# Kernel optimization log

Hardware: AMD Instinct MI355X
Metric: run time of the kernel (lower is better)

The kernel has to match this reference:

```python
import jax, jax.numpy as jnp
import numpy as np

N = 100000
E = 3200000
D_IN = 128
D_OUT = 128


def setup_inputs() -> dict:
    key = jax.random.key(0)
    k1, k2, k3, k4, k5, k6, k7 = jax.random.split(key, 7)
    stdv = 1.0 / np.sqrt(D_OUT)
    x = jax.random.normal(k1, (N, D_IN), dtype=jnp.float32)
    rows = jax.random.randint(k2, (E,), 0, N, dtype=jnp.int32)
    cols = jax.random.randint(k3, (E,), 0, N, dtype=jnp.int32)
    edge_w = jax.random.uniform(k4, (E,), dtype=jnp.float32)
    W = jax.random.uniform(k5, (D_IN, D_OUT), minval=-stdv, maxval=stdv, dtype=jnp.float32)
    W_skip = jax.random.uniform(k6, (D_IN, D_OUT), minval=-stdv, maxval=stdv, dtype=jnp.float32)
    b = jax.random.uniform(k7, (D_OUT,), minval=-stdv, maxval=stdv, dtype=jnp.float32)
    return {"x": x, "rows": rows, "cols": cols, "edge_w": edge_w,
            "W": W, "W_skip": W_skip, "b": b}


def reference(x, rows, cols, edge_w, W, W_skip, b):
    # support1 = x @ W  [N, D_OUT]
    support1 = jnp.dot(x, W)
    # spmm(norm_adj, support1): out[r] = sum_{(r,c) in E} w_rc * support1[c]
    msgs = support1[cols] * edge_w[:, None]          # [E, D_OUT] gather
    agg = jax.ops.segment_sum(msgs, rows, num_segments=N)  # [N, D_OUT] scatter-add
    # skip connection + bias
    out = agg + jnp.dot(x, W_skip) + b
    return out
```

## Files before the change

kernel.cpp:

```cpp
#include <hip/hip_runtime.h>

#define D 128
#define B_LOG 6
#define ROWS_PB 64
#define MAX_NB 2048
#define GEMM_GRID 784
#define CHUNK_LOG 12
#define CAP 2560

typedef short bf16x8 __attribute__((ext_vector_type(8)));
typedef float f32x4  __attribute__((ext_vector_type(4)));

static __device__ __forceinline__ unsigned short f2bf(float f) {
    unsigned u = __float_as_uint(f);
    u += 0x7FFFu + ((u >> 16) & 1u);
    return (unsigned short)(u >> 16);
}

__global__ __launch_bounds__(256) void wconv_kernel(
    const float* __restrict__ W, const float* __restrict__ Ws,
    short* __restrict__ Wt, int* __restrict__ bhist, int nb)
{
    const int idx = blockIdx.x * 256 + threadIdx.x;
    if (idx < 2 * D * D) {
        const int mat = idx >> 14;
        const int rem = idx & (D * D - 1);
        const int n = rem >> 7, k = rem & (D - 1);
        const float* src = mat ? Ws : W;
        Wt[idx] = (short)f2bf(src[k * D + n]);
    }
    if (idx < nb) bhist[idx] = 0;
}

__global__ __launch_bounds__(256) void bhist_kernel(
    const int* __restrict__ rows, int* __restrict__ bhist, int E, int nb)
{
    __shared__ int h[MAX_NB];
    const int t = threadIdx.x;
    for (int i = t; i < nb; i += 256) h[i] = 0;
    __syncthreads();

    int i = blockIdx.x * 256 + t;
    const int stride = gridDim.x * 256;
    for (; i < E; i += stride) atomicAdd(&h[rows[i] >> B_LOG], 1);
    __syncthreads();

    for (int i2 = t; i2 < nb; i2 += 256) {
        const int c = h[i2];
        if (c) atomicAdd(&bhist[i2], c);
    }
}

__global__ __launch_bounds__(256) void bscan_kernel(
    const int* __restrict__ bhist, int* __restrict__ bptr,
    int* __restrict__ bcur, int nb)
{
    const int t = threadIdx.x;
    const int base_i = t * 8;
    int v[8];
    int s = 0;
#pragma unroll
    for (int k = 0; k < 8; ++k) {
        v[k] = (base_i + k < nb) ? bhist[base_i + k] : 0;
        s += v[k];
    }

    const int lane = t & 63, wv = t >> 6;
    int sc = s;
    for (int o = 1; o < 64; o <<= 1) {
        const int u = __shfl_up(sc, o, 64);
        if (lane >= o) sc += u;
    }
    __shared__ int wsum[4];
    if (lane == 63) wsum[wv] = sc;
    __syncthreads();

    int wbase = 0;
    for (int w2 = 0; w2 < wv; ++w2) wbase += wsum[w2];
    int excl = wbase + (sc - s);
#pragma unroll
    for (int k = 0; k < 8; ++k) {
        if (base_i + k < nb) { bptr[base_i + k] = excl; bcur[base_i + k] = excl; }
        excl += v[k];
    }
    if (t == 255) bptr[nb] = wsum[0] + wsum[1] + wsum[2] + wsum[3];
}

__global__ __launch_bounds__(256) void gemm_part_kernel(
    const float* __restrict__ x, const short* __restrict__ Wt,
    const float* __restrict__ b, unsigned short* __restrict__ s1b,
    unsigned short* __restrict__ skipb, int N,
    const int* __restrict__ rows, const int* __restrict__ cols,
    const float* __restrict__ ew, int* __restrict__ bcur,
    int2* __restrict__ se1, int E, int nb)
{
    __shared__ short sx[64 * D];

    const int t = threadIdx.x;

    if (blockIdx.x >= GEMM_GRID) {
        int* h = (int*)sx;
        const int nbl = gridDim.x - GEMM_GRID;
        const int nchunks = (E + (1 << CHUNK_LOG) - 1) >> CHUNK_LOG;

        for (int c = blockIdx.x - GEMM_GRID; c < nchunks; c += nbl) {
            const int ebeg = c << CHUNK_LOG;
            const int eend = min(ebeg + (1 << CHUNK_LOG), E);

            for (int i = t; i < nb; i += 256) h[i] = 0;
            __syncthreads();

            for (int e = ebeg + t; e < eend; e += 256)
                atomicAdd(&h[rows[e] >> B_LOG], 1);
            __syncthreads();

            for (int i = t; i < nb; i += 256) {
                const int cnt = h[i];
                h[i] = cnt ? atomicAdd(&bcur[i], cnt) : 0;
            }
            __syncthreads();

            for (int e = ebeg + t; e < eend; e += 256) {
                const int r    = rows[e];
                const int bkt  = r >> B_LOG;
                const int slot = atomicAdd(&h[bkt], 1);
                se1[slot] = make_int2(((r & (ROWS_PB - 1)) << 20) | cols[e],
                                      __float_as_int(ew[e]));
            }
            __syncthreads();
        }
        return;
    }

    const int lane = t & 63;
    const int w    = t >> 6;

    const int bmat = w >> 1;
    const int bn0  = (w & 1) * 64 + (lane & 15);
    const int bk0  = (lane >> 4) * 8;
    bf16x8 Bf[4][4];
#pragma unroll
    for (int nf = 0; nf < 4; ++nf)
#pragma unroll
        for (int ks = 0; ks < 4; ++ks)
            Bf[nf][ks] = *(const bf16x8*)&Wt[
                ((size_t)bmat * D + bn0 + nf * 16) * D + ks * 32 + bk0];

    float bias[4];
#pragma unroll
    for (int nf = 0; nf < 4; ++nf)
        bias[nf] = (w >= 2) ? b[(w - 2) * 64 + nf * 16 + (lane & 15)] : 0.f;

    const int ntiles = (N + 63) >> 6;
    const int trow = t >> 2;
    const int tk   = (t & 3) * 4;

    for (int rt = blockIdx.x; rt < ntiles; rt += GEMM_GRID) {
        const int r0 = rt << 6;
        __syncthreads();

        const int grow = min(r0 + trow, N - 1);
        const float* xrow = &x[(size_t)grow * D];
#pragma unroll
        for (int i = 0; i < 8; ++i) {
            const int k = tk + i * 16;
            const float4 v = *(const float4*)&xrow[k];
            const unsigned lo = (unsigned)f2bf(v.x) | ((unsigned)f2bf(v.y) << 16);
            const unsigned hi = (unsigned)f2bf(v.z) | ((unsigned)f2bf(v.w) << 16);
            unsigned byte = trow * 256 + k * 2;
            byte ^= (unsigned)((trow & 7) << 4);
            *(uint2*)((char*)sx + byte) = make_uint2(lo, hi);
        }
        __syncthreads();

        f32x4 acc[4][4];
#pragma unroll
        for (int mf = 0; mf < 4; ++mf)
#pragma unroll
            for (int nf = 0; nf < 4; ++nf)
                acc[mf][nf] = (f32x4){0.f, 0.f, 0.f, 0.f};

#pragma unroll
        for (int ks = 0; ks < 4; ++ks) {
            bf16x8 Af[4];
#pragma unroll
            for (int mf = 0; mf < 4; ++mf) {
                const int row = mf * 16 + (lane & 15);
                unsigned byte = row * 256 + (ks * 32 + bk0) * 2;
                byte ^= (unsigned)((row & 7) << 4);
                Af[mf] = *(const bf16x8*)((const char*)sx + byte);
            }
#pragma unroll
            for (int mf = 0; mf < 4; ++mf)
#pragma unroll
                for (int nf = 0; nf < 4; ++nf)
                    acc[mf][nf] = __builtin_amdgcn_mfma_f32_16x16x32_bf16(
                        Af[mf], Bf[nf][ks], acc[mf][nf], 0, 0, 0);
        }

#pragma unroll
        for (int mf = 0; mf < 4; ++mf) {
#pragma unroll
            for (int i = 0; i < 4; ++i) {
                const int row = r0 + mf * 16 + (lane >> 4) * 4 + i;
                if (row < N) {
                    if (w < 2) {
#pragma unroll
                        for (int nf = 0; nf < 4; ++nf) {
                            const int col = w * 64 + nf * 16 + (lane & 15);
                            s1b[(size_t)row * D + col] = f2bf(acc[mf][nf][i]);
                        }
                    } else {
#pragma unroll
                        for (int nf = 0; nf < 4; ++nf) {
                            const int col = (w - 2) * 64 + nf * 16 + (lane & 15);
                            skipb[(size_t)row * D + col] =
                                f2bf(acc[mf][nf][i] + bias[nf]);
                        }
                    }
                }
            }
        }
    }
}

__global__ __launch_bounds__(512) void sortspmm_kernel(
    const unsigned short* __restrict__ s1b,
    const unsigned short* __restrict__ skipb,
    const int* __restrict__ bptr, const int2* __restrict__ se1,
    float* __restrict__ out, int N)
{
    __shared__ long long recs[CAP];
    __shared__ int rpos[ROWS_PB];
    __shared__ int rcur[ROWS_PB];

    const int t    = threadIdx.x;
    const int lane = t & 63;
    const int wv   = t >> 6;
    const int bk   = blockIdx.x;
    const int r0   = bk << B_LOG;
    const int j    = lane * 2;

    const int beg  = bptr[bk];
    const int end  = bptr[bk + 1];
    const int cntE = end - beg;
    const long long* seq = (const long long*)se1;

    if (t < ROWS_PB) rcur[t] = 0;
    __syncthreads();

    for (int e = beg + t; e < end; e += 512)
        atomicAdd(&rcur[(unsigned)se1[e].x >> 20], 1);
    __syncthreads();

    if (t < ROWS_PB) rpos[t] = rcur[t];
    __syncthreads();
#pragma unroll
    for (int off = 1; off < ROWS_PB; off <<= 1) {
        int v = (t < ROWS_PB && t >= off) ? rpos[t - off] : 0;
        __syncthreads();
        if (t < ROWS_PB) rpos[t] += v;
        __syncthreads();
    }
    if (t < ROWS_PB) {
        const int excl = rpos[t] - rcur[t];
        rpos[t] = excl;
        rcur[t] = excl;
    }
    __syncthreads();

    if (cntE <= CAP) {
        for (int e = beg + t; e < end; e += 512) {
            const long long rec = seq[e];
            const int rl = (int)((unsigned)rec >> 20);
            const int slot = atomicAdd(&rcur[rl], 1);
            recs[slot] = rec;
        }
        __syncthreads();

        for (int i = 0; i < 8; ++i) {
            const int rr = wv * 8 + i;
            const int r  = r0 + rr;
            if (r >= N) break;
            int p        = rpos[rr];
            const int pe = rcur[rr];

            float2 acc = make_float2(0.f, 0.f);
            for (; p + 8 <= pe; p += 8) {
                long long ed[8];
#pragma unroll
                for (int k = 0; k < 8; ++k) ed[k] = recs[p + k];
                unsigned pk[8];
#pragma unroll
                for (int k = 0; k < 8; ++k)
                    pk[k] = *(const unsigned*)&s1b[
                        (size_t)((unsigned)ed[k] & 0xFFFFFu) * D + j];
#pragma unroll
                for (int k = 0; k < 8; ++k) {
                    const float w = __int_as_float((int)(ed[k] >> 32));
                    acc.x = fmaf(w, __uint_as_float(pk[k] << 16), acc.x);
                    acc.y = fmaf(w, __uint_as_float(pk[k] & 0xFFFF0000u), acc.y);
                }
            }
            for (; p < pe; ++p) {
                const long long ed = recs[p];
                const unsigned pk = *(const unsigned*)&s1b[
                    (size_t)((unsigned)ed & 0xFFFFFu) * D + j];
                const float w = __int_as_float((int)(ed >> 32));
                acc.x = fmaf(w, __uint_as_float(pk << 16), acc.x);
                acc.y = fmaf(w, __uint_as_float(pk & 0xFFFF0000u), acc.y);
            }

            const unsigned sk = *(const unsigned*)&skipb[(size_t)r * D + j];
            float2 o;
            o.x = acc.x + __uint_as_float(sk << 16);
            o.y = acc.y + __uint_as_float(sk & 0xFFFF0000u);
            *(float2*)&out[(size_t)r * D + j] = o;
        }
    } else {
        const int nr = min(ROWS_PB, N - r0);
        for (int idx = t; idx < nr * 64; idx += 512) {
            const int rr = idx >> 6;
            const int cc = (idx & 63) * 2;
            const unsigned sk = *(const unsigned*)&skipb[(size_t)(r0 + rr) * D + cc];
            *(float2*)&out[(size_t)(r0 + rr) * D + cc] =
                make_float2(__uint_as_float(sk << 16),
                            __uint_as_float(sk & 0xFFFF0000u));
        }
        __syncthreads();

        for (int e = beg + wv; e < end; e += 8) {
            const long long ed = seq[e];
            const unsigned key = (unsigned)ed;
            const int rl = (int)(key >> 20);
            const float w = __int_as_float((int)(ed >> 32));
            const unsigned pk = *(const unsigned*)&s1b[
                (size_t)(key & 0xFFFFFu) * D + j];
            float* op = &out[(size_t)(r0 + rl) * D + j];
            unsafeAtomicAdd(op,     w * __uint_as_float(pk << 16));
            unsafeAtomicAdd(op + 1, w * __uint_as_float(pk & 0xFFFF0000u));
        }
    }
}

__global__ __launch_bounds__(512) void dual_gemm_fb_kernel(
    const float* __restrict__ x, const float* __restrict__ W,
    const float* __restrict__ Ws, const float* __restrict__ b,
    unsigned short* __restrict__ s1b, float* __restrict__ out, int N)
{
    __shared__ float sW[D * D];
    __shared__ float sWs[D * D];

    const int t = threadIdx.x;
    for (int i = t * 4; i < D * D; i += 512 * 4) {
        *(float4*)&sW[i]  = *(const float4*)&W[i];
        *(float4*)&sWs[i] = *(const float4*)&Ws[i];
    }
    __syncthreads();

    const int lane   = t & 63;
    const int wave   = blockIdx.x * 8 + (t >> 6);
    const int nwaves = gridDim.x * 8;
    const int j      = lane * 2;
    const float2 bb  = *(const float2*)&b[j];

    for (int r0 = wave * 4; r0 < N; r0 += nwaves * 4) {
        float2 xr[4];
#pragma unroll
        for (int r = 0; r < 4; ++r)
            xr[r] = *(const float2*)&x[(size_t)(r0 + r) * D + j];

        float2 a1[4], a2[4];
#pragma unroll
        for (int r = 0; r < 4; ++r) {
            a1[r] = make_float2(0.f, 0.f);
            a2[r] = make_float2(0.f, 0.f);
        }

#pragma unroll 8
        for (int k = 0; k < D; ++k) {
            const float2 wk  = *(const float2*)&sW[k * D + j];
            const float2 wsk = *(const float2*)&sWs[k * D + j];
#pragma unroll
            for (int r = 0; r < 4; ++r) {
                const float xv = __shfl((k & 1) ? xr[r].y : xr[r].x, k >> 1, 64);
                a1[r].x = fmaf(xv, wk.x,  a1[r].x);
                a1[r].y = fmaf(xv, wk.y,  a1[r].y);
                a2[r].x = fmaf(xv, wsk.x, a2[r].x);
                a2[r].y = fmaf(xv, wsk.y, a2[r].y);
            }
        }

#pragma unroll
        for (int r = 0; r < 4; ++r) {
            const unsigned pk = (unsigned)f2bf(a1[r].x) |
                                ((unsigned)f2bf(a1[r].y) << 16);
            *(unsigned*)&s1b[(size_t)(r0 + r) * D + j] = pk;
            *(float2*)&out[(size_t)(r0 + r) * D + j] =
                make_float2(a2[r].x + bb.x, a2[r].y + bb.y);
        }
    }
}

__global__ __launch_bounds__(256) void spmm_edges_kernel(
    const unsigned short* __restrict__ s1b, const int* __restrict__ rows,
    const int* __restrict__ cols, const float* __restrict__ ew,
    float* __restrict__ out, int E)
{
    const int lane = threadIdx.x & 63;
    const int wave = blockIdx.x * (blockDim.x >> 6) + (threadIdx.x >> 6);
    const int nw   = gridDim.x * (blockDim.x >> 6);
    const int j    = lane * 2;

    const int epw   = (E + nw - 1) / nw;
    const int e_beg = wave * epw;
    const int e_end = min(e_beg + epw, E);

    for (int e = e_beg; e < e_end; ++e) {
        const int   r = rows[e];
        const int   c = cols[e];
        const float w = ew[e];
        const unsigned p = *(const unsigned*)&s1b[(size_t)c * D + j];
        float* o = &out[(size_t)r * D + j];
        unsafeAtomicAdd(o,     w * __uint_as_float(p << 16));
        unsafeAtomicAdd(o + 1, w * __uint_as_float(p & 0xFFFF0000u));
    }
}

extern "C" void kernel_launch(void* const* d_in, const int* in_sizes, int n_in,
                              void* d_out, int out_size, void* d_ws, size_t ws_size,
                              hipStream_t stream) {
    const float* x    = (const float*)d_in[0];
    const int*   rows = (const int*)  d_in[1];
    const int*   cols = (const int*)  d_in[2];
    const float* ew   = (const float*)d_in[3];
    const float* W    = (const float*)d_in[4];
    const float* Ws   = (const float*)d_in[5];
    const float* b    = (const float*)d_in[6];
    float*       out  = (float*)d_out;

    const int N  = in_sizes[0] / D;
    const int E  = in_sizes[1];
    const int nb = (N + ROWS_PB - 1) >> B_LOG;

    const size_t s1_bytes   = ((size_t)N * D * 2 + 15) & ~(size_t)15;
    const size_t skip_bytes = s1_bytes;
    const size_t wt_bytes   = (size_t)2 * D * D * 2;
    const size_t int_bytes  = (((size_t)(3 * nb + 1)) * 4 + 7) & ~(size_t)7;
    const size_t need       = s1_bytes + skip_bytes + wt_bytes + int_bytes
                              + (size_t)E * 8;

    unsigned short* s1b = (unsigned short*)d_ws;

    if (ws_size >= need && nb <= MAX_NB) {
        unsigned short* skipb = (unsigned short*)((char*)d_ws + s1_bytes);
        short* Wt    = (short*)((char*)d_ws + s1_bytes + skip_bytes);
        int*   ibase = (int*)((char*)d_ws + s1_bytes + skip_bytes + wt_bytes);
        int*  bhist  = ibase;
        int*  bptr   = ibase + nb;
        int*  bcur   = ibase + 2 * nb + 1;
        int2* se1    = (int2*)((char*)d_ws + s1_bytes + skip_bytes + wt_bytes
                               + int_bytes);

        wconv_kernel<<<(2 * D * D + 255) / 256, 256, 0, stream>>>(W, Ws, Wt, bhist, nb);
        bhist_kernel<<<512, 256, 0, stream>>>(rows, bhist, E, nb);
        bscan_kernel<<<1, 256, 0, stream>>>(bhist, bptr, bcur, nb);

        const int nchunks = (E + (1 << CHUNK_LOG) - 1) >> CHUNK_LOG;
        const int part_blocks = min(nchunks, 1024);
        gemm_part_kernel<<<GEMM_GRID + part_blocks, 256, 0, stream>>>(
            x, Wt, b, s1b, skipb, N, rows, cols, ew, bcur, se1, E, nb);

        sortspmm_kernel<<<nb, 512, 0, stream>>>(s1b, skipb, bptr, se1, out, N);
    } else {
        dual_gemm_fb_kernel<<<768, 512, 0, stream>>>(x, W, Ws, b, s1b, (float*)d_out, N);
        spmm_edges_kernel<<<2048, 256, 0, stream>>>(s1b, rows, cols, ew, (float*)d_out, E);
    }
}
```

Measured before the change: 225.4 us.

## Partition edges into 128-row buckets, split each bucket across two SpMM blocks

Edge bucketing now uses 128 rows per bucket, which halves the bucket count and shrinks the shared-memory histogram and scatter work in the partition phase. Each SpMM bucket is processed by two blocks, each handling one 64-row half and filtering out records for the other half. The per-block row prefix scan is replaced by a single-wave shuffle scan. The cost is that each SpMM block reads its whole 128-row bucket's records twice (count pass and placement pass), so global record traffic in the SpMM kernel roughly doubles.

```diff
diff --git a/kernel.cpp b/kernel.cpp
--- a/kernel.cpp
+++ b/kernel.cpp
@@ -1,9 +1,9 @@
 #include <hip/hip_runtime.h>
 
 #define D 128
-#define B_LOG 6
-#define ROWS_PB 64
-#define MAX_NB 2048
+#define BP_LOG 7
+#define ROWS_H 64
+#define MAX_NB 1024
 #define GEMM_GRID 784
 #define CHUNK_LOG 12
 #define CAP 2560
@@ -42,7 +42,7 @@
 
     int i = blockIdx.x * 256 + t;
     const int stride = gridDim.x * 256;
-    for (; i < E; i += stride) atomicAdd(&h[rows[i] >> B_LOG], 1);
+    for (; i < E; i += stride) atomicAdd(&h[rows[i] >> BP_LOG], 1);
     __syncthreads();
 
     for (int i2 = t; i2 < nb; i2 += 256) {
@@ -56,11 +56,11 @@
     int* __restrict__ bcur, int nb)
 {
     const int t = threadIdx.x;
-    const int base_i = t * 8;
-    int v[8];
+    const int base_i = t * 4;
+    int v[4];
     int s = 0;
 #pragma unroll
-    for (int k = 0; k < 8; ++k) {
+    for (int k = 0; k < 4; ++k) {
         v[k] = (base_i + k < nb) ? bhist[base_i + k] : 0;
         s += v[k];
     }
@@ -79,7 +79,7 @@
     for (int w2 = 0; w2 < wv; ++w2) wbase += wsum[w2];
     int excl = wbase + (sc - s);
 #pragma unroll
-    for (int k = 0; k < 8; ++k) {
+    for (int k = 0; k < 4; ++k) {
         if (base_i + k < nb) { bptr[base_i + k] = excl; bcur[base_i + k] = excl; }
         excl += v[k];
     }
@@ -111,7 +111,7 @@
             __syncthreads();
 
             for (int e = ebeg + t; e < eend; e += 256)
-                atomicAdd(&h[rows[e] >> B_LOG], 1);
+                atomicAdd(&h[rows[e] >> BP_LOG], 1);
             __syncthreads();
 
             for (int i = t; i < nb; i += 256) {
@@ -122,9 +122,9 @@
 
             for (int e = ebeg + t; e < eend; e += 256) {
                 const int r    = rows[e];
-                const int bkt  = r >> B_LOG;
+                const int bkt  = r >> BP_LOG;
                 const int slot = atomicAdd(&h[bkt], 1);
-                se1[slot] = make_int2(((r & (ROWS_PB - 1)) << 20) | cols[e],
+                se1[slot] = make_int2(((r & 127) << 20) | cols[e],
                                       __float_as_int(ew[e]));
             }
             __syncthreads();
@@ -231,50 +231,54 @@
     float* __restrict__ out, int N)
 {
     __shared__ long long recs[CAP];
-    __shared__ int rpos[ROWS_PB];
-    __shared__ int rcur[ROWS_PB];
+    __shared__ int rpos[ROWS_H];
+    __shared__ int rcur[ROWS_H];
+    __shared__ int hcnt_s;
 
     const int t    = threadIdx.x;
     const int lane = t & 63;
     const int wv   = t >> 6;
-    const int bk   = blockIdx.x;
-    const int r0   = bk << B_LOG;
+    const int sb   = blockIdx.x >> 1;
+    const int hh   = blockIdx.x & 1;
+    const int r0   = (sb << BP_LOG) + (hh << 6);
     const int j    = lane * 2;
 
-    const int beg  = bptr[bk];
-    const int end  = bptr[bk + 1];
-    const int cntE = end - beg;
+    const int beg  = bptr[sb];
+    const int end  = bptr[sb + 1];
     const long long* seq = (const long long*)se1;
 
-    if (t < ROWS_PB) rcur[t] = 0;
-    __syncthreads();
-
-    for (int e = beg + t; e < end; e += 512)
-        atomicAdd(&rcur[(unsigned)se1[e].x >> 20], 1);
-    __syncthreads();
-
-    if (t < ROWS_PB) rpos[t] = rcur[t];
-    __syncthreads();
-#pragma unroll
-    for (int off = 1; off < ROWS_PB; off <<= 1) {
-        int v = (t < ROWS_PB && t >= off) ? rpos[t - off] : 0;
-        __syncthreads();
-        if (t < ROWS_PB) rpos[t] += v;
-        __syncthreads();
-    }
-    if (t < ROWS_PB) {
-        const int excl = rpos[t] - rcur[t];
-        rpos[t] = excl;
-        rcur[t] = excl;
-    }
-    __syncthreads();
-
-    if (cntE <= CAP) {
+    if (t < ROWS_H) rcur[t] = 0;
+    __syncthreads();
+
+    for (int e = beg + t; e < end; e += 512) {
+        const int rl = (int)((unsigned)se1[e].x >> 20);
+        if ((rl >> 6) == hh) atomicAdd(&rcur[rl & 63], 1);
+    }
+    __syncthreads();
+
+    if (t < ROWS_H) {
+        const int v = rcur[t];
+        int sc = v;
+#pragma unroll
+        for (int o = 1; o < 64; o <<= 1) {
+            const int u = __shfl_up(sc, o, 64);
+            if (lane >= o) sc += u;
+        }
+        rpos[t] = sc - v;
+        rcur[t] = sc - v;
+        if (t == 63) hcnt_s = sc;
+    }
+    __syncthreads();
+    const int hcnt = hcnt_s;
+
+    if (hcnt <= CAP) {
         for (int e = beg + t; e < end; e += 512) {
             const long long rec = seq[e];
             const int rl = (int)((unsigned)rec >> 20);
-            const int slot = atomicAdd(&rcur[rl], 1);
-            recs[slot] = rec;
+            if ((rl >> 6) == hh) {
+                const int slot = atomicAdd(&rcur[rl & 63], 1);
+                recs[slot] = rec;
+            }
         }
         __syncthreads();
 
@@ -318,7 +322,7 @@
             *(float2*)&out[(size_t)r * D + j] = o;
         }
     } else {
-        const int nr = min(ROWS_PB, N - r0);
+        const int nr = min(ROWS_H, N - r0);
         for (int idx = t; idx < nr * 64; idx += 512) {
             const int rr = idx >> 6;
             const int cc = (idx & 63) * 2;
@@ -333,10 +337,11 @@
             const long long ed = seq[e];
             const unsigned key = (unsigned)ed;
             const int rl = (int)(key >> 20);
+            if ((rl >> 6) != hh) continue;
             const float w = __int_as_float((int)(ed >> 32));
             const unsigned pk = *(const unsigned*)&s1b[
                 (size_t)(key & 0xFFFFFu) * D + j];
-            float* op = &out[(size_t)(r0 + rl) * D + j];
+            float* op = &out[(size_t)(r0 + (rl & 63)) * D + j];
             unsafeAtomicAdd(op,     w * __uint_as_float(pk << 16));
             unsafeAtomicAdd(op + 1, w * __uint_as_float(pk & 0xFFFF0000u));
         }
@@ -441,7 +446,7 @@
 
     const int N  = in_sizes[0] / D;
     const int E  = in_sizes[1];
-    const int nb = (N + ROWS_PB - 1) >> B_LOG;
+    const int nb = (N + 127) >> BP_LOG;
 
     const size_t s1_bytes   = ((size_t)N * D * 2 + 15) & ~(size_t)15;
     const size_t skip_bytes = s1_bytes;
@@ -471,7 +476,7 @@
         gemm_part_kernel<<<GEMM_GRID + part_blocks, 256, 0, stream>>>(
             x, Wt, b, s1b, skipb, N, rows, cols, ew, bcur, se1, E, nb);
 
-        sortspmm_kernel<<<nb, 512, 0, stream>>>(s1b, skipb, bptr, se1, out, N);
+        sortspmm_kernel<<<nb * 2, 512, 0, stream>>>(s1b, skipb, bptr, se1, out, N);
     } else {
         dual_gemm_fb_kernel<<<768, 512, 0, stream>>>(x, W, Ws, b, s1b, (float*)d_out, N);
         spmm_edges_kernel<<<2048, 256, 0, stream>>>(s1b, rows, cols, ew, (float*)d_out, E);
```

Result: faster. 219.7 us (-2.6%).
